# Kernel tuning notes

Hardware: AMD Instinct MI355X
Metric: run time of the kernel (lower is better)

Reference implementation:

```python
import math
import jax, jax.numpy as jnp
import numpy as np

NT, NS, B, D, V = 128, 128, 8, 512, 32000


def setup_inputs() -> dict:
    key = jax.random.key(0)
    ks = jax.random.split(key, 9)
    s = 0.02
    return {
        "htgt": jax.random.normal(ks[0], (NT, B, D), jnp.float32),
        "hsrc": jax.random.normal(ks[1], (NS, B, D), jnp.float32),
        "src": jax.random.randint(ks[2], (NS, B), 0, V),
        "Wq": jax.random.normal(ks[3], (D, D), jnp.float32) * s,
        "bq": jnp.zeros((D,), jnp.float32),
        "Wf": jax.random.normal(ks[4], (D, D), jnp.float32) * s,
        "bf": jnp.zeros((D,), jnp.float32),
        "Wg": jax.random.normal(ks[5], (D, V), jnp.float32) * s,
        "bg": jnp.zeros((V,), jnp.float32),
        "Wc": jax.random.normal(ks[6], (D, 1), jnp.float32) * s,
        "bc": jnp.zeros((1,), jnp.float32),
    }


def reference(htgt, hsrc, src, Wq, bq, Wf, bf, Wg, bg, Wc, bc):
    Nt, bs, d = htgt.shape
    vocab = Wg.shape[1]
    # generator logits: (Nt,B,V) -> (B,Nt,V)
    p_gen = (jnp.einsum('tbd,dv->tbv', htgt, Wg) + bg).transpose(1, 0, 2)
    # single-head attention; NOTE: original code projects q, k, v all with q_proj
    q = (htgt @ Wq + bq).transpose(1, 0, 2) / math.sqrt(d)   # (B,Nt,D)
    k = (hsrc @ Wq + bq).transpose(1, 0, 2)                  # (B,Ns,D)
    v = (hsrc @ Wq + bq).transpose(1, 0, 2)                  # (B,Ns,D)
    attn = jax.nn.softmax(jnp.einsum('btd,bsd->bts', q, k), axis=-1)  # (B,Nt,Ns)
    x = jnp.einsum('bts,bsd->btd', attn, v)                  # (B,Nt,D)
    scores = x @ Wf + bf                                     # (B,Nt,D)
    # copy gate: sum over target positions (original sums dim 0 of (Nt,B,D))
    a_copy = jax.nn.sigmoid(scores.sum(axis=1) @ Wc + bc)    # (B,1)
    a_copy = a_copy[:, :, None]                              # (B,1,1)
    # scatter-add attention probs into vocab buckets (replaces one-hot bmm)
    def scat(attn_b, src_b):
        return jnp.zeros((attn_b.shape[0], vocab), attn_b.dtype).at[:, src_b].add(attn_b)
    p_copy = jax.vmap(scat)(attn, src.T)                     # (B,Nt,V)
    res = a_copy * p_copy + (1.0 - a_copy) * p_gen           # (B,Nt,V)
    return res.transpose(1, 0, 2)                            # (Nt,B,V)
```

## Files before the change

kernel.cpp:

```cpp
#include <hip/hip_runtime.h>
#include <math.h>

#define NTt 128
#define NSs 128
#define BB  8
#define DD  512
#define VV  32000

typedef unsigned short ushortT;
typedef unsigned int uintT;
__device__ __forceinline__ ushortT f2bf(float x) {
    uintT u = __float_as_uint(x);
    u = (u + 0x7fffu + ((u >> 16) & 1u)) >> 16;
    return (ushortT)u;
}
__device__ __forceinline__ float bf2f(ushortT h) {
    return __uint_as_float(((uintT)h) << 16);
}

typedef __attribute__((ext_vector_type(8))) short bf16x8;
typedef __attribute__((ext_vector_type(4))) float f32x4;

__global__ __launch_bounds__(256)
void wfc_kernel(const float* __restrict__ Wf, const float* __restrict__ Wc,
                float* __restrict__ wfc) {
    __shared__ float sWc[DD];
    const int tid = threadIdx.x;
    sWc[tid] = Wc[tid];
    sWc[tid + 256] = Wc[tid + 256];
    __syncthreads();
    const int w = tid >> 6, lane = tid & 63;
    const int row = blockIdx.x * 4 + w;
    const float* r = Wf + (size_t)row * DD + lane * 8;
    float4 a = *(const float4*)r;
    float4 b = *(const float4*)(r + 4);
    const float* c = &sWc[lane * 8];
    float s = a.x * c[0] + a.y * c[1] + a.z * c[2] + a.w * c[3]
            + b.x * c[4] + b.y * c[5] + b.z * c[6] + b.w * c[7];
    for (int off = 32; off; off >>= 1) s += __shfl_xor(s, off);
    if (lane == 0) wfc[row] = s;
}

#define QBM 64
#define QBN 64
#define QBK 16
__global__ __launch_bounds__(256)
void qkv_gemm(const float* __restrict__ htgt, const float* __restrict__ hsrc,
              const float* __restrict__ Wq, const float* __restrict__ bq,
              float* __restrict__ QK) {
    __shared__ float As[QBK][QBM];
    __shared__ float Bs[QBK][QBN];
    const int m0 = blockIdx.x * QBM;
    const int n0 = blockIdx.y * QBN;
    const int tid = threadIdx.x;
    const int tx = tid & 15, ty = tid >> 4;
    const float* Abase = (m0 < 1024) ? (htgt + (size_t)m0 * DD)
                                     : (hsrc + (size_t)(m0 - 1024) * DD);
    float acc[4][4];
#pragma unroll
    for (int i = 0; i < 4; ++i)
#pragma unroll
        for (int j = 0; j < 4; ++j) acc[i][j] = 0.f;

    const int ar = tid >> 2;
    const int ak = (tid & 3) * 4;
    const int br = tid >> 4;
    const int bc4 = (tid & 15) * 4;

    for (int k0 = 0; k0 < DD; k0 += QBK) {
        float4 av = *(const float4*)(Abase + (size_t)ar * DD + k0 + ak);
        float4 bv = *(const float4*)(Wq + (size_t)(k0 + br) * DD + n0 + bc4);
        As[ak + 0][ar] = av.x; As[ak + 1][ar] = av.y;
        As[ak + 2][ar] = av.z; As[ak + 3][ar] = av.w;
        *(float4*)&Bs[br][bc4] = bv;
        __syncthreads();
#pragma unroll
        for (int kk = 0; kk < QBK; ++kk) {
            float4 a4 = *(const float4*)&As[kk][ty * 4];
            float4 b4 = *(const float4*)&Bs[kk][tx * 4];
            float a[4] = {a4.x, a4.y, a4.z, a4.w};
            float b[4] = {b4.x, b4.y, b4.z, b4.w};
#pragma unroll
            for (int i = 0; i < 4; ++i)
#pragma unroll
                for (int j = 0; j < 4; ++j)
                    acc[i][j] = fmaf(a[i], b[j], acc[i][j]);
        }
        __syncthreads();
    }
    const float scale = (m0 < 1024) ? 0.044194173824159216f : 1.0f;
    float4 bqv = *(const float4*)&bq[n0 + tx * 4];
#pragma unroll
    for (int i = 0; i < 4; ++i) {
        const int m = m0 + ty * 4 + i;
        float4 o;
        o.x = (acc[i][0] + bqv.x) * scale;
        o.y = (acc[i][1] + bqv.y) * scale;
        o.z = (acc[i][2] + bqv.z) * scale;
        o.w = (acc[i][3] + bqv.w) * scale;
        *(float4*)&QK[(size_t)m * DD + n0 + tx * 4] = o;
    }
}

__global__ __launch_bounds__(256)
void attn_kernel(const float* __restrict__ QK, float* __restrict__ attn,
                 float* __restrict__ colsum) {
    const int b = blockIdx.x & 7;
    const int tpair = blockIdx.x >> 3;
    const int tid = threadIdx.x;
    const int h = tid >> 7;
    const int s = tid & 127;
    const int t = tpair * 2 + h;
    __shared__ float sQ[2][DD];
    __shared__ float sred[8];
    sQ[h][s * 4 + 0] = 0.f;
    *(float4*)&sQ[h][s * 4] = *(const float4*)&QK[(size_t)(t * BB + b) * DD + s * 4];
    __syncthreads();
    const float* Krow = QK + (size_t)(1024 + s * BB + b) * DD;
    const float* q = &sQ[h][0];
    float4 accv = make_float4(0.f, 0.f, 0.f, 0.f);
    for (int d = 0; d < DD; d += 4) {
        float4 kv = *(const float4*)(Krow + d);
        accv.x = fmaf(kv.x, q[d + 0], accv.x);
        accv.y = fmaf(kv.y, q[d + 1], accv.y);
        accv.z = fmaf(kv.z, q[d + 2], accv.z);
        accv.w = fmaf(kv.w, q[d + 3], accv.w);
    }
    const float dot = accv.x + accv.y + accv.z + accv.w;
    float m = dot;
    for (int off = 32; off; off >>= 1) m = fmaxf(m, __shfl_xor(m, off));
    const int wv = tid >> 6;
    if ((tid & 63) == 0) sred[wv] = m;
    __syncthreads();
    m = fmaxf(sred[h * 2], sred[h * 2 + 1]);
    const float p = __expf(dot - m);
    float ssum = p;
    for (int off = 32; off; off >>= 1) ssum += __shfl_xor(ssum, off);
    __syncthreads();
    if ((tid & 63) == 0) sred[4 + wv] = ssum;
    __syncthreads();
    ssum = sred[4 + h * 2] + sred[4 + h * 2 + 1];
    const float a = p / ssum;
    attn[(size_t)(b * NTt + t) * NSs + s] = a;
    atomicAdd(&colsum[b * NSs + s], a);
}

__global__ __launch_bounds__(128)
void acopy_kernel(const float* __restrict__ QK, const float* __restrict__ wfc,
                  const float* __restrict__ colsum, const float* __restrict__ bf,
                  const float* __restrict__ Wc, const float* __restrict__ bc,
                  float* __restrict__ ac) {
    const int b = blockIdx.x;
    const int tid = threadIdx.x;
    __shared__ float sW[DD];
    __shared__ float sred[4];
    *(float4*)&sW[tid * 4] = *(const float4*)&wfc[tid * 4];
    __syncthreads();
    const float* Krow = QK + (size_t)(1024 + tid * BB + b) * DD;
    float4 accv = make_float4(0.f, 0.f, 0.f, 0.f);
    for (int d = 0; d < DD; d += 4) {
        float4 kv = *(const float4*)(Krow + d);
        accv.x = fmaf(kv.x, sW[d + 0], accv.x);
        accv.y = fmaf(kv.y, sW[d + 1], accv.y);
        accv.z = fmaf(kv.z, sW[d + 2], accv.z);
        accv.w = fmaf(kv.w, sW[d + 3], accv.w);
    }
    const float kw = accv.x + accv.y + accv.z + accv.w;
    float val = colsum[b * NSs + tid] * kw;
    float cw = 0.f;
#pragma unroll
    for (int j = 0; j < 4; ++j) cw += bf[tid + j * 128] * Wc[tid + j * 128];
    for (int off = 32; off; off >>= 1) {
        val += __shfl_xor(val, off);
        cw  += __shfl_xor(cw, off);
    }
    if ((tid & 63) == 0) { sred[tid >> 6] = val; sred[2 + (tid >> 6)] = cw; }
    __syncthreads();
    if (tid == 0) {
        const float z = sred[0] + sred[1] + (float)NTt * (sred[2] + sred[3]) + bc[0];
        ac[b] = 1.0f / (1.0f + __expf(-z));
    }
}

__global__ __launch_bounds__(256)
void split_prep(const float* __restrict__ Wg, const float* __restrict__ htgt,
                ushortT* __restrict__ Bh, ushortT* __restrict__ Bl,
                ushortT* __restrict__ Ah, ushortT* __restrict__ Al) {
    __shared__ float tile[32][65];
    const int bx = blockIdx.x;
    const int tid = threadIdx.x;
    if (bx < 8000) {
        const int n0 = (bx % 500) * 64;
        const int k0 = (bx / 500) * 32;
        for (int c = tid; c < 512; c += 256) {
            const int r = c >> 4;
            const int q = (c & 15) * 4;
            float4 v = *(const float4*)(Wg + (size_t)(k0 + r) * VV + n0 + q);
            tile[r][q + 0] = v.x; tile[r][q + 1] = v.y;
            tile[r][q + 2] = v.z; tile[r][q + 3] = v.w;
        }
        __syncthreads();
        const int n = tid >> 2;
        const int ks = (tid & 3) * 8;
        uintT h[8], l[8];
#pragma unroll
        for (int j = 0; j < 8; ++j) {
            const float x = tile[ks + j][n];
            h[j] = f2bf(x);
            l[j] = f2bf(x - bf2f((ushortT)h[j]));
        }
        uint4 hv, lv;
        hv.x = h[0] | (h[1] << 16); hv.y = h[2] | (h[3] << 16);
        hv.z = h[4] | (h[5] << 16); hv.w = h[6] | (h[7] << 16);
        lv.x = l[0] | (l[1] << 16); lv.y = l[2] | (l[3] << 16);
        lv.z = l[4] | (l[5] << 16); lv.w = l[6] | (l[7] << 16);
        const size_t ob = (size_t)(n0 + n) * 512 + k0 + ks;
        *(uint4*)(Bh + ob) = hv;
        *(uint4*)(Bl + ob) = lv;
    } else {
        const int gid = (bx - 8000) * 256 + tid;
        const size_t base = (size_t)gid * 8;
        float4 v0 = *(const float4*)(htgt + base);
        float4 v1 = *(const float4*)(htgt + base + 4);
        float x[8] = {v0.x, v0.y, v0.z, v0.w, v1.x, v1.y, v1.z, v1.w};
        uintT h[8], l[8];
#pragma unroll
        for (int i = 0; i < 8; ++i) {
            h[i] = f2bf(x[i]);
            l[i] = f2bf(x[i] - bf2f((ushortT)h[i]));
        }
        uint4 hv, lv;
        hv.x = h[0] | (h[1] << 16); hv.y = h[2] | (h[3] << 16);
        hv.z = h[4] | (h[5] << 16); hv.w = h[6] | (h[7] << 16);
        lv.x = l[0] | (l[1] << 16); lv.y = l[2] | (l[3] << 16);
        lv.z = l[4] | (l[5] << 16); lv.w = l[6] | (l[7] << 16);
        *(uint4*)(Ah + base) = hv;
        *(uint4*)(Al + base) = lv;
    }
}

#define PK  32
#define PKP 40
__global__ __launch_bounds__(256)
void pgen_mfma(const ushortT* __restrict__ Ah, const ushortT* __restrict__ Al,
               const ushortT* __restrict__ Bh, const ushortT* __restrict__ Bl,
               const float* __restrict__ bg, const float* __restrict__ ac,
               float* __restrict__ out) {
    __shared__ __align__(16) ushortT sAh[128][PKP];
    __shared__ __align__(16) ushortT sAl[128][PKP];
    __shared__ __align__(16) ushortT sBh[128][PKP];
    __shared__ __align__(16) ushortT sBl[128][PKP];
    __shared__ float s_ac[8];

    const int idx = blockIdx.x;
    const int wg  = (idx & 7) * 250 + (idx >> 3);
    const int nb  = wg >> 3;
    const int mb  = wg & 7;
    const int m0 = mb * 128;
    const int n0 = nb * 128;

    const int tid = threadIdx.x;
    const int wid = tid >> 6;
    const int lane = tid & 63;
    const int wm = wid >> 1, wn = wid & 1;
    const int g = lane >> 4;
    const int lr = lane & 15;

    if (tid < 8) s_ac[tid] = 1.0f - ac[tid];

    f32x4 acc[4][4];
#pragma unroll
    for (int i = 0; i < 4; ++i)
#pragma unroll
        for (int j = 0; j < 4; ++j) acc[i][j] = (f32x4){0.f, 0.f, 0.f, 0.f};

    for (int k0 = 0; k0 < DD; k0 += PK) {
#pragma unroll
        for (int c8 = 0; c8 < 8; ++c8) {
            const int c = tid + c8 * 256;
            const int ab = c >> 10;
            const int cc = c & 1023;
            const int row = cc >> 3;
            const int mat = (cc >> 2) & 1;
            const int part = cc & 3;
            const ushortT* src;
            ushortT* dst;
            if (ab == 0) {
                src = (mat ? Al : Ah) + (size_t)(m0 + row) * 512 + k0 + part * 8;
                dst = (mat ? &sAl[0][0] : &sAh[0][0]) + row * PKP + part * 8;
            } else {
                src = (mat ? Bl : Bh) + (size_t)(n0 + row) * 512 + k0 + part * 8;
                dst = (mat ? &sBl[0][0] : &sBh[0][0]) + row * PKP + part * 8;
            }
            *(uint4*)dst = *(const uint4*)src;
        }
        __syncthreads();

        bf16x8 fah[4], fal[4], fbh[4], fbl[4];
#pragma unroll
        for (int i = 0; i < 4; ++i) {
            fah[i] = *(const bf16x8*)&sAh[wm * 64 + i * 16 + lr][g * 8];
            fal[i] = *(const bf16x8*)&sAl[wm * 64 + i * 16 + lr][g * 8];
            fbh[i] = *(const bf16x8*)&sBh[wn * 64 + i * 16 + lr][g * 8];
            fbl[i] = *(const bf16x8*)&sBl[wn * 64 + i * 16 + lr][g * 8];
        }
#pragma unroll
        for (int mi = 0; mi < 4; ++mi)
#pragma unroll
            for (int ni = 0; ni < 4; ++ni) {
                acc[mi][ni] = __builtin_amdgcn_mfma_f32_16x16x32_bf16(
                    fah[mi], fbh[ni], acc[mi][ni], 0, 0, 0);
                acc[mi][ni] = __builtin_amdgcn_mfma_f32_16x16x32_bf16(
                    fah[mi], fbl[ni], acc[mi][ni], 0, 0, 0);
                acc[mi][ni] = __builtin_amdgcn_mfma_f32_16x16x32_bf16(
                    fal[mi], fbh[ni], acc[mi][ni], 0, 0, 0);
            }
        __syncthreads();
    }

    float bgv[4];
#pragma unroll
    for (int i = 0; i < 4; ++i) bgv[i] = bg[n0 + wn * 64 + i * 16 + lr];
#pragma unroll
    for (int mi = 0; mi < 4; ++mi) {
#pragma unroll
        for (int r = 0; r < 4; ++r) {
            const int m = m0 + wm * 64 + mi * 16 + g * 4 + r;
            const float s = s_ac[(g * 4 + r) & 7];
            const size_t ob = (size_t)m * VV + n0 + wn * 64 + lr;
#pragma unroll
            for (int ni = 0; ni < 4; ++ni) {
                out[ob + ni * 16] = s * (acc[mi][ni][r] + bgv[ni]);
            }
        }
    }
}

#define BM 128
#define BN 128
#define BK 8
__global__ __launch_bounds__(256)
void pgen_gemm(const float* __restrict__ htgt, const float* __restrict__ Wg,
               const float* __restrict__ bg, const float* __restrict__ ac,
               float* __restrict__ out) {
    __shared__ float As[BK][BM];
    __shared__ float Bs[BK][BN];
    const int m0 = blockIdx.x * BM;
    const int n0 = blockIdx.y * BN;
    const int tid = threadIdx.x;
    const int tx = tid & 15, ty = tid >> 4;
    const float* Abase = htgt + (size_t)m0 * DD;
    float acc[8][8];
#pragma unroll
    for (int i = 0; i < 8; ++i)
#pragma unroll
        for (int j = 0; j < 8; ++j) acc[i][j] = 0.f;
    const int ar = tid >> 1;
    const int ah = (tid & 1) * 4;
    const int bk = tid >> 5;
    const int bj = (tid & 31) * 4;
    for (int k0 = 0; k0 < DD; k0 += BK) {
        float4 av = *(const float4*)(Abase + (size_t)ar * DD + k0 + ah);
        float4 bv = *(const float4*)(Wg + (size_t)(k0 + bk) * VV + n0 + bj);
        As[ah + 0][ar] = av.x; As[ah + 1][ar] = av.y;
        As[ah + 2][ar] = av.z; As[ah + 3][ar] = av.w;
        *(float4*)&Bs[bk][bj] = bv;
        __syncthreads();
#pragma unroll
        for (int kk = 0; kk < BK; ++kk) {
            float4 a0 = *(const float4*)&As[kk][ty * 8];
            float4 a1 = *(const float4*)&As[kk][ty * 8 + 4];
            float4 b0 = *(const float4*)&Bs[kk][tx * 8];
            float4 b1 = *(const float4*)&Bs[kk][tx * 8 + 4];
            float a[8] = {a0.x, a0.y, a0.z, a0.w, a1.x, a1.y, a1.z, a1.w};
            float b[8] = {b0.x, b0.y, b0.z, b0.w, b1.x, b1.y, b1.z, b1.w};
#pragma unroll
            for (int i = 0; i < 8; ++i)
#pragma unroll
                for (int j = 0; j < 8; ++j)
                    acc[i][j] = fmaf(a[i], b[j], acc[i][j]);
        }
        __syncthreads();
    }
    float sc[8];
#pragma unroll
    for (int i = 0; i < 8; ++i) sc[i] = 1.0f - ac[i];
#pragma unroll
    for (int i = 0; i < 8; ++i) {
        const int m = m0 + ty * 8 + i;
        const float s = sc[i];
#pragma unroll
        for (int j = 0; j < 8; j += 4) {
            const int n = n0 + tx * 8 + j;
            float4 o;
            o.x = s * (acc[i][j + 0] + bg[n + 0]);
            o.y = s * (acc[i][j + 1] + bg[n + 1]);
            o.z = s * (acc[i][j + 2] + bg[n + 2]);
            o.w = s * (acc[i][j + 3] + bg[n + 3]);
            *(float4*)&out[(size_t)m * VV + n] = o;
        }
    }
}

__global__ __launch_bounds__(256)
void scatter_kernel(const float* __restrict__ attn, const float* __restrict__ ac,
                    const int* __restrict__ src, float* __restrict__ out) {
    const int gid = blockIdx.x * 256 + threadIdx.x;
    const int b = gid >> 14;
    const int rem = gid & 16383;
    const int t = rem >> 7;
    const int s = rem & 127;
    const float a = ac[b];
    const int v = src[s * BB + b];
    atomicAdd(&out[(size_t)(t * BB + b) * VV + v],
              a * attn[(size_t)(b * NTt + t) * NSs + s]);
}

extern "C" void kernel_launch(void* const* d_in, const int* in_sizes, int n_in,
                              void* d_out, int out_size, void* d_ws, size_t ws_size,
                              hipStream_t stream) {
    (void)in_sizes; (void)n_in; (void)out_size;
    const float* htgt = (const float*)d_in[0];
    const float* hsrc = (const float*)d_in[1];
    const int*   src  = (const int*)d_in[2];
    const float* Wq   = (const float*)d_in[3];
    const float* bq   = (const float*)d_in[4];
    const float* Wf   = (const float*)d_in[5];
    const float* bf   = (const float*)d_in[6];
    const float* Wg   = (const float*)d_in[7];
    const float* bg   = (const float*)d_in[8];
    const float* Wc   = (const float*)d_in[9];
    const float* bc   = (const float*)d_in[10];
    float* out = (float*)d_out;

    float* ws     = (float*)d_ws;
    float* QK     = ws;
    float* attn   = QK + 2048 * 512;
    float* colsum = attn + 131072;
    float* wfc    = colsum + 1024;
    float* ac     = wfc + 512;

    size_t fp32_bytes = (size_t)(1048576 + 131072 + 1024 + 512 + 16) * 4;
    size_t base2 = (fp32_bytes + 255) & ~(size_t)255;
    ushortT* Ah = (ushortT*)((char*)d_ws + base2);
    ushortT* Al = Ah + (size_t)1024 * 512;
    ushortT* Bh = Al + (size_t)1024 * 512;
    ushortT* Bl = Bh + (size_t)32000 * 512;
    size_t need = base2 + 2 * (size_t)1024 * 512 * 2 + 2 * (size_t)32000 * 512 * 2;

    hipMemsetAsync(colsum, 0, 1024 * sizeof(float), stream);
    wfc_kernel<<<128, 256, 0, stream>>>(Wf, Wc, wfc);
    if (ws_size >= need) {
        split_prep<<<8256, 256, 0, stream>>>(Wg, htgt, Bh, Bl, Ah, Al);
    }
    qkv_gemm<<<dim3(32, 8), 256, 0, stream>>>(htgt, hsrc, Wq, bq, QK);
    attn_kernel<<<512, 256, 0, stream>>>(QK, attn, colsum);
    acopy_kernel<<<8, 128, 0, stream>>>(QK, wfc, colsum, bf, Wc, bc, ac);

    if (ws_size >= need) {
        pgen_mfma<<<2000, 256, 0, stream>>>(Ah, Al, Bh, Bl, bg, ac, out);
    } else {
        pgen_gemm<<<dim3(8, 250), 256, 0, stream>>>(htgt, Wg, bg, ac, out);
    }
    scatter_kernel<<<512, 256, 0, stream>>>(attn, ac, src, out);
}
```

Before: 427.5 us.

## Prepack bf16 split tiles for direct global-to-LDS loads and drop colsum atomics

The prep kernel now writes the Wg and htgt hi/lo bf16 splits in a pre-tiled layout of 128x32 blocks, and the wfc computation is merged into the same launch. This lets pgen_mfma fill shared memory with global_load_lds 16-byte copies instead of staging through registers with per-element index math. The atomic colsum accumulation and its memset are removed, and acopy_kernel now sums attention columns itself. In exchange, the unpadded 32-element LDS rows may cause bank conflicts on fragment reads. The fallback path launches prep_kernel with only 128 blocks, which would run the Wg-packing branch into the float workspace and never compute wfc.

```diff
diff --git a/kernel.cpp b/kernel.cpp
--- a/kernel.cpp
+++ b/kernel.cpp
@@ -21,24 +21,101 @@
 typedef __attribute__((ext_vector_type(8))) short bf16x8;
 typedef __attribute__((ext_vector_type(4))) float f32x4;
 
-__global__ __launch_bounds__(256)
-void wfc_kernel(const float* __restrict__ Wf, const float* __restrict__ Wc,
-                float* __restrict__ wfc) {
-    __shared__ float sWc[DD];
-    const int tid = threadIdx.x;
-    sWc[tid] = Wc[tid];
-    sWc[tid + 256] = Wc[tid + 256];
-    __syncthreads();
-    const int w = tid >> 6, lane = tid & 63;
-    const int row = blockIdx.x * 4 + w;
-    const float* r = Wf + (size_t)row * DD + lane * 8;
-    float4 a = *(const float4*)r;
-    float4 b = *(const float4*)(r + 4);
-    const float* c = &sWc[lane * 8];
-    float s = a.x * c[0] + a.y * c[1] + a.z * c[2] + a.w * c[3]
-            + b.x * c[4] + b.y * c[5] + b.z * c[6] + b.w * c[7];
-    for (int off = 32; off; off >>= 1) s += __shfl_xor(s, off);
-    if (lane == 0) wfc[row] = s;
+#define GLL16(g, l) __builtin_amdgcn_global_load_lds(                          \
+    (const __attribute__((address_space(1))) unsigned int*)(g),                \
+    (__attribute__((address_space(3))) unsigned int*)(l), 16, 0, 0)
+
+#define LDSC 4096
+
+__global__ __launch_bounds__(256)
+void prep_kernel(const float* __restrict__ Wg, const float* __restrict__ htgt,
+                 const float* __restrict__ Wf, const float* __restrict__ Wc,
+                 ushortT* __restrict__ Bpack, ushortT* __restrict__ Apack,
+                 float* __restrict__ wfc) {
+    const int bx = blockIdx.x;
+    const int tid = threadIdx.x;
+    if (bx < 4000) {
+        __shared__ float tile[32][129];
+        const int p = bx >> 4, t = bx & 15;
+        const int n0 = p * 128, k0 = t * 32;
+#pragma unroll
+        for (int i = 0; i < 4; ++i) {
+            const int idx = tid + i * 256;
+            const int row = idx >> 5;
+            const int c4 = (idx & 31) * 4;
+            float4 v = *(const float4*)(Wg + (size_t)(k0 + row) * VV + n0 + c4);
+            tile[row][c4 + 0] = v.x; tile[row][c4 + 1] = v.y;
+            tile[row][c4 + 2] = v.z; tile[row][c4 + 3] = v.w;
+        }
+        __syncthreads();
+        const int r = tid >> 1;
+        const int c2 = tid & 1;
+        uintT h[16], l[16];
+#pragma unroll
+        for (int j = 0; j < 16; ++j) {
+            const float x = tile[c2 * 16 + j][r];
+            h[j] = f2bf(x);
+            l[j] = f2bf(x - bf2f((ushortT)h[j]));
+        }
+        ushortT* dh = Bpack + ((size_t)(p * 16 + t) * 2 + 0) * LDSC + r * 32 + c2 * 16;
+        ushortT* dl = Bpack + ((size_t)(p * 16 + t) * 2 + 1) * LDSC + r * 32 + c2 * 16;
+        uint4 hv0, hv1, lv0, lv1;
+        hv0.x = h[0] | (h[1] << 16);  hv0.y = h[2] | (h[3] << 16);
+        hv0.z = h[4] | (h[5] << 16);  hv0.w = h[6] | (h[7] << 16);
+        hv1.x = h[8] | (h[9] << 16);  hv1.y = h[10] | (h[11] << 16);
+        hv1.z = h[12] | (h[13] << 16); hv1.w = h[14] | (h[15] << 16);
+        lv0.x = l[0] | (l[1] << 16);  lv0.y = l[2] | (l[3] << 16);
+        lv0.z = l[4] | (l[5] << 16);  lv0.w = l[6] | (l[7] << 16);
+        lv1.x = l[8] | (l[9] << 16);  lv1.y = l[10] | (l[11] << 16);
+        lv1.z = l[12] | (l[13] << 16); lv1.w = l[14] | (l[15] << 16);
+        *(uint4*)dh = hv0; *(uint4*)(dh + 8) = hv1;
+        *(uint4*)dl = lv0; *(uint4*)(dl + 8) = lv1;
+    } else if (bx < 4128) {
+        const int idx = bx - 4000;
+        const int p = idx >> 4, t = idx & 15;
+        const int r = tid >> 1, c2 = tid & 1;
+        const float* srcp = htgt + (size_t)(p * 128 + r) * DD + t * 32 + c2 * 16;
+        uintT h[16], l[16];
+#pragma unroll
+        for (int q = 0; q < 4; ++q) {
+            float4 v = *(const float4*)(srcp + q * 4);
+            float xs[4] = {v.x, v.y, v.z, v.w};
+#pragma unroll
+            for (int j = 0; j < 4; ++j) {
+                const int e = q * 4 + j;
+                h[e] = f2bf(xs[j]);
+                l[e] = f2bf(xs[j] - bf2f((ushortT)h[e]));
+            }
+        }
+        ushortT* dh = Apack + ((size_t)(p * 16 + t) * 2 + 0) * LDSC + r * 32 + c2 * 16;
+        ushortT* dl = Apack + ((size_t)(p * 16 + t) * 2 + 1) * LDSC + r * 32 + c2 * 16;
+        uint4 hv0, hv1, lv0, lv1;
+        hv0.x = h[0] | (h[1] << 16);  hv0.y = h[2] | (h[3] << 16);
+        hv0.z = h[4] | (h[5] << 16);  hv0.w = h[6] | (h[7] << 16);
+        hv1.x = h[8] | (h[9] << 16);  hv1.y = h[10] | (h[11] << 16);
+        hv1.z = h[12] | (h[13] << 16); hv1.w = h[14] | (h[15] << 16);
+        lv0.x = l[0] | (l[1] << 16);  lv0.y = l[2] | (l[3] << 16);
+        lv0.z = l[4] | (l[5] << 16);  lv0.w = l[6] | (l[7] << 16);
+        lv1.x = l[8] | (l[9] << 16);  lv1.y = l[10] | (l[11] << 16);
+        lv1.z = l[12] | (l[13] << 16); lv1.w = l[14] | (l[15] << 16);
+        *(uint4*)dh = hv0; *(uint4*)(dh + 8) = hv1;
+        *(uint4*)dl = lv0; *(uint4*)(dl + 8) = lv1;
+    } else {
+        __shared__ float sWc[DD];
+        sWc[tid] = Wc[tid];
+        sWc[tid + 256] = Wc[tid + 256];
+        __syncthreads();
+        const int w = tid >> 6, lane = tid & 63;
+        const int row = (bx - 4128) * 4 + w;
+        const float* rp = Wf + (size_t)row * DD + lane * 8;
+        float4 a = *(const float4*)rp;
+        float4 b = *(const float4*)(rp + 4);
+        const float* c = &sWc[lane * 8];
+        float s = a.x * c[0] + a.y * c[1] + a.z * c[2] + a.w * c[3]
+                + b.x * c[4] + b.y * c[5] + b.z * c[6] + b.w * c[7];
+        for (int off = 32; off; off >>= 1) s += __shfl_xor(s, off);
+        if (lane == 0) wfc[row] = s;
+    }
 }
 
 #define QBM 64
@@ -103,8 +180,7 @@
 }
 
 __global__ __launch_bounds__(256)
-void attn_kernel(const float* __restrict__ QK, float* __restrict__ attn,
-                 float* __restrict__ colsum) {
+void attn_kernel(const float* __restrict__ QK, float* __restrict__ attn) {
     const int b = blockIdx.x & 7;
     const int tpair = blockIdx.x >> 3;
     const int tid = threadIdx.x;
@@ -113,7 +189,6 @@
     const int t = tpair * 2 + h;
     __shared__ float sQ[2][DD];
     __shared__ float sred[8];
-    sQ[h][s * 4 + 0] = 0.f;
     *(float4*)&sQ[h][s * 4] = *(const float4*)&QK[(size_t)(t * BB + b) * DD + s * 4];
     __syncthreads();
     const float* Krow = QK + (size_t)(1024 + s * BB + b) * DD;
@@ -140,14 +215,12 @@
     if ((tid & 63) == 0) sred[4 + wv] = ssum;
     __syncthreads();
     ssum = sred[4 + h * 2] + sred[4 + h * 2 + 1];
-    const float a = p / ssum;
-    attn[(size_t)(b * NTt + t) * NSs + s] = a;
-    atomicAdd(&colsum[b * NSs + s], a);
+    attn[(size_t)(b * NTt + t) * NSs + s] = p / ssum;
 }
 
 __global__ __launch_bounds__(128)
 void acopy_kernel(const float* __restrict__ QK, const float* __restrict__ wfc,
-                  const float* __restrict__ colsum, const float* __restrict__ bf,
+                  const float* __restrict__ attn, const float* __restrict__ bf,
                   const float* __restrict__ Wc, const float* __restrict__ bc,
                   float* __restrict__ ac) {
     const int b = blockIdx.x;
@@ -156,6 +229,10 @@
     __shared__ float sred[4];
     *(float4*)&sW[tid * 4] = *(const float4*)&wfc[tid * 4];
     __syncthreads();
+    float cs = 0.f;
+    const float* arow = attn + (size_t)b * NTt * NSs + tid;
+#pragma unroll 4
+    for (int tq = 0; tq < NTt; ++tq) cs += arow[(size_t)tq * NSs];
     const float* Krow = QK + (size_t)(1024 + tid * BB + b) * DD;
     float4 accv = make_float4(0.f, 0.f, 0.f, 0.f);
     for (int d = 0; d < DD; d += 4) {
@@ -166,7 +243,7 @@
         accv.w = fmaf(kv.w, sW[d + 3], accv.w);
     }
     const float kw = accv.x + accv.y + accv.z + accv.w;
-    float val = colsum[b * NSs + tid] * kw;
+    float val = cs * kw;
     float cw = 0.f;
 #pragma unroll
     for (int j = 0; j < 4; ++j) cw += bf[tid + j * 128] * Wc[tid + j * 128];
@@ -183,73 +260,10 @@
 }
 
 __global__ __launch_bounds__(256)
-void split_prep(const float* __restrict__ Wg, const float* __restrict__ htgt,
-                ushortT* __restrict__ Bh, ushortT* __restrict__ Bl,
-                ushortT* __restrict__ Ah, ushortT* __restrict__ Al) {
-    __shared__ float tile[32][65];
-    const int bx = blockIdx.x;
-    const int tid = threadIdx.x;
-    if (bx < 8000) {
-        const int n0 = (bx % 500) * 64;
-        const int k0 = (bx / 500) * 32;
-        for (int c = tid; c < 512; c += 256) {
-            const int r = c >> 4;
-            const int q = (c & 15) * 4;
-            float4 v = *(const float4*)(Wg + (size_t)(k0 + r) * VV + n0 + q);
-            tile[r][q + 0] = v.x; tile[r][q + 1] = v.y;
-            tile[r][q + 2] = v.z; tile[r][q + 3] = v.w;
-        }
-        __syncthreads();
-        const int n = tid >> 2;
-        const int ks = (tid & 3) * 8;
-        uintT h[8], l[8];
-#pragma unroll
-        for (int j = 0; j < 8; ++j) {
-            const float x = tile[ks + j][n];
-            h[j] = f2bf(x);
-            l[j] = f2bf(x - bf2f((ushortT)h[j]));
-        }
-        uint4 hv, lv;
-        hv.x = h[0] | (h[1] << 16); hv.y = h[2] | (h[3] << 16);
-        hv.z = h[4] | (h[5] << 16); hv.w = h[6] | (h[7] << 16);
-        lv.x = l[0] | (l[1] << 16); lv.y = l[2] | (l[3] << 16);
-        lv.z = l[4] | (l[5] << 16); lv.w = l[6] | (l[7] << 16);
-        const size_t ob = (size_t)(n0 + n) * 512 + k0 + ks;
-        *(uint4*)(Bh + ob) = hv;
-        *(uint4*)(Bl + ob) = lv;
-    } else {
-        const int gid = (bx - 8000) * 256 + tid;
-        const size_t base = (size_t)gid * 8;
-        float4 v0 = *(const float4*)(htgt + base);
-        float4 v1 = *(const float4*)(htgt + base + 4);
-        float x[8] = {v0.x, v0.y, v0.z, v0.w, v1.x, v1.y, v1.z, v1.w};
-        uintT h[8], l[8];
-#pragma unroll
-        for (int i = 0; i < 8; ++i) {
-            h[i] = f2bf(x[i]);
-            l[i] = f2bf(x[i] - bf2f((ushortT)h[i]));
-        }
-        uint4 hv, lv;
-        hv.x = h[0] | (h[1] << 16); hv.y = h[2] | (h[3] << 16);
-        hv.z = h[4] | (h[5] << 16); hv.w = h[6] | (h[7] << 16);
-        lv.x = l[0] | (l[1] << 16); lv.y = l[2] | (l[3] << 16);
-        lv.z = l[4] | (l[5] << 16); lv.w = l[6] | (l[7] << 16);
-        *(uint4*)(Ah + base) = hv;
-        *(uint4*)(Al + base) = lv;
-    }
-}
-
-#define PK  32
-#define PKP 40
-__global__ __launch_bounds__(256)
-void pgen_mfma(const ushortT* __restrict__ Ah, const ushortT* __restrict__ Al,
-               const ushortT* __restrict__ Bh, const ushortT* __restrict__ Bl,
+void pgen_mfma(const ushortT* __restrict__ Apack, const ushortT* __restrict__ Bpack,
                const float* __restrict__ bg, const float* __restrict__ ac,
                float* __restrict__ out) {
-    __shared__ __align__(16) ushortT sAh[128][PKP];
-    __shared__ __align__(16) ushortT sAl[128][PKP];
-    __shared__ __align__(16) ushortT sBh[128][PKP];
-    __shared__ __align__(16) ushortT sBl[128][PKP];
+    __shared__ __align__(16) ushortT sT[4 * LDSC];
     __shared__ float s_ac[8];
 
     const int idx = blockIdx.x;
@@ -268,41 +282,33 @@
 
     if (tid < 8) s_ac[tid] = 1.0f - ac[tid];
 
+    const ushortT* gsrc = ((wid < 2) ? (Apack + (size_t)mb * 16 * 2 * LDSC)
+                                     : (Bpack + (size_t)nb * 16 * 2 * LDSC))
+                          + (size_t)(wid & 1) * LDSC;
+    ushortT* ldst = &sT[wid * LDSC];
+
     f32x4 acc[4][4];
 #pragma unroll
     for (int i = 0; i < 4; ++i)
 #pragma unroll
         for (int j = 0; j < 4; ++j) acc[i][j] = (f32x4){0.f, 0.f, 0.f, 0.f};
 
-    for (int k0 = 0; k0 < DD; k0 += PK) {
-#pragma unroll
-        for (int c8 = 0; c8 < 8; ++c8) {
-            const int c = tid + c8 * 256;
-            const int ab = c >> 10;
-            const int cc = c & 1023;
-            const int row = cc >> 3;
-            const int mat = (cc >> 2) & 1;
-            const int part = cc & 3;
-            const ushortT* src;
-            ushortT* dst;
-            if (ab == 0) {
-                src = (mat ? Al : Ah) + (size_t)(m0 + row) * 512 + k0 + part * 8;
-                dst = (mat ? &sAl[0][0] : &sAh[0][0]) + row * PKP + part * 8;
-            } else {
-                src = (mat ? Bl : Bh) + (size_t)(n0 + row) * 512 + k0 + part * 8;
-                dst = (mat ? &sBl[0][0] : &sBh[0][0]) + row * PKP + part * 8;
-            }
-            *(uint4*)dst = *(const uint4*)src;
+    for (int t = 0; t < 16; ++t) {
+#pragma unroll
+        for (int i = 0; i < 8; ++i) {
+            GLL16(gsrc + i * 512 + lane * 8, ldst + i * 512);
         }
         __syncthreads();
 
         bf16x8 fah[4], fal[4], fbh[4], fbl[4];
 #pragma unroll
         for (int i = 0; i < 4; ++i) {
-            fah[i] = *(const bf16x8*)&sAh[wm * 64 + i * 16 + lr][g * 8];
-            fal[i] = *(const bf16x8*)&sAl[wm * 64 + i * 16 + lr][g * 8];
-            fbh[i] = *(const bf16x8*)&sBh[wn * 64 + i * 16 + lr][g * 8];
-            fbl[i] = *(const bf16x8*)&sBl[wn * 64 + i * 16 + lr][g * 8];
+            const int arow = wm * 64 + i * 16 + lr;
+            const int brow = wn * 64 + i * 16 + lr;
+            fah[i] = *(const bf16x8*)&sT[0 * LDSC + arow * 32 + g * 8];
+            fal[i] = *(const bf16x8*)&sT[1 * LDSC + arow * 32 + g * 8];
+            fbh[i] = *(const bf16x8*)&sT[2 * LDSC + brow * 32 + g * 8];
+            fbl[i] = *(const bf16x8*)&sT[3 * LDSC + brow * 32 + g * 8];
         }
 #pragma unroll
         for (int mi = 0; mi < 4; ++mi)
@@ -316,6 +322,7 @@
                     fal[mi], fbh[ni], acc[mi][ni], 0, 0, 0);
             }
         __syncthreads();
+        gsrc += 2 * LDSC;
     }
 
     float bgv[4];
@@ -433,32 +440,31 @@
     const float* bc   = (const float*)d_in[10];
     float* out = (float*)d_out;
 
-    float* ws     = (float*)d_ws;
-    float* QK     = ws;
-    float* attn   = QK + 2048 * 512;
-    float* colsum = attn + 131072;
-    float* wfc    = colsum + 1024;
-    float* ac     = wfc + 512;
-
-    size_t fp32_bytes = (size_t)(1048576 + 131072 + 1024 + 512 + 16) * 4;
+    float* ws   = (float*)d_ws;
+    float* QK   = ws;
+    float* attn = QK + 2048 * 512;
+    float* wfc  = attn + 131072;
+    float* ac   = wfc + 512;
+
+    size_t fp32_bytes = (size_t)(1048576 + 131072 + 512 + 16) * 4;
     size_t base2 = (fp32_bytes + 255) & ~(size_t)255;
-    ushortT* Ah = (ushortT*)((char*)d_ws + base2);
-    ushortT* Al = Ah + (size_t)1024 * 512;
-    ushortT* Bh = Al + (size_t)1024 * 512;
-    ushortT* Bl = Bh + (size_t)32000 * 512;
-    size_t need = base2 + 2 * (size_t)1024 * 512 * 2 + 2 * (size_t)32000 * 512 * 2;
-
-    hipMemsetAsync(colsum, 0, 1024 * sizeof(float), stream);
-    wfc_kernel<<<128, 256, 0, stream>>>(Wf, Wc, wfc);
-    if (ws_size >= need) {
-        split_prep<<<8256, 256, 0, stream>>>(Wg, htgt, Bh, Bl, Ah, Al);
+    ushortT* Apack = (ushortT*)((char*)d_ws + base2);
+    ushortT* Bpack = Apack + (size_t)8 * 16 * 2 * LDSC;
+    size_t need = base2 + ((size_t)8 * 16 * 2 * LDSC + (size_t)250 * 16 * 2 * LDSC) * 2;
+
+    const bool use_mfma = (ws_size >= need);
+    if (use_mfma) {
+        prep_kernel<<<4256, 256, 0, stream>>>(Wg, htgt, Wf, Wc, Bpack, Apack, wfc);
+    } else {
+        prep_kernel<<<dim3(128), 256, 0, stream>>>(Wg, htgt, Wf, Wc,
+                                                   (ushortT*)ws, (ushortT*)ws, wfc);
     }
     qkv_gemm<<<dim3(32, 8), 256, 0, stream>>>(htgt, hsrc, Wq, bq, QK);
-    attn_kernel<<<512, 256, 0, stream>>>(QK, attn, colsum);
-    acopy_kernel<<<8, 128, 0, stream>>>(QK, wfc, colsum, bf, Wc, bc, ac);
-
-    if (ws_size >= need) {
-        pgen_mfma<<<2000, 256, 0, stream>>>(Ah, Al, Bh, Bl, bg, ac, out);
+    attn_kernel<<<512, 256, 0, stream>>>(QK, attn);
+    acopy_kernel<<<8, 128, 0, stream>>>(QK, wfc, attn, bf, Wc, bc, ac);
+
+    if (use_mfma) {
+        pgen_mfma<<<2000, 256, 0, stream>>>(Apack, Bpack, bg, ac, out);
     } else {
         pgen_gemm<<<dim3(8, 250), 256, 0, stream>>>(htgt, Wg, bg, ac, out);
     }
```

After: 411.3 us. -3.8%, faster.
